# Kernel optimization log

Hardware: AMD Instinct MI355X
Metric: run time of the kernel (lower is better)

## Reference

```python
import jax, jax.numpy as jnp
import numpy as np

N_NODES = 100000
N_EDGES = 600000
DIM = 128
N_BEHAVIORS = 4


def setup_inputs() -> dict:
    key = jax.random.key(0)
    ks = jax.random.split(key, 10)
    user = jax.random.randint(ks[0], (N_NODES,), 0, N_NODES, dtype=jnp.int32)
    item = jax.random.randint(ks[1], (N_NODES,), 0, N_NODES, dtype=jnp.int32)
    behavior = jax.random.randint(ks[2], (N_NODES,), 0, N_BEHAVIORS, dtype=jnp.int32)
    adj_rows = jax.random.randint(ks[3], (N_EDGES,), 0, N_NODES, dtype=jnp.int32)
    adj_cols = jax.random.randint(ks[4], (N_EDGES,), 0, N_NODES, dtype=jnp.int32)
    adj_vals = jax.random.uniform(ks[5], (N_EDGES,), dtype=jnp.float32)
    user_table = jax.random.normal(ks[6], (N_NODES, DIM), dtype=jnp.float32)
    item_table = jax.random.normal(ks[7], (N_NODES, DIM), dtype=jnp.float32)
    behavior_table = jax.random.normal(ks[8], (N_BEHAVIORS, DIM), dtype=jnp.float32)
    kw, kb = jax.random.split(ks[9])
    bound = 1.0 / np.sqrt(DIM)
    W = jax.random.uniform(kw, (DIM, DIM), minval=-bound, maxval=bound, dtype=jnp.float32)
    b = jax.random.uniform(kb, (DIM,), minval=-bound, maxval=bound, dtype=jnp.float32)
    return {"user": user, "item": item, "behavior": behavior,
            "adj_rows": adj_rows, "adj_cols": adj_cols, "adj_vals": adj_vals,
            "user_table": user_table, "item_table": item_table,
            "behavior_table": behavior_table, "W": W, "b": b}


def reference(user, item, behavior, adj_rows, adj_cols, adj_vals,
              user_table, item_table, behavior_table, W, b):
    # embedding sum: [N, D]
    x = user_table[user] + item_table[item] + behavior_table[behavior]
    # sparse adjacency matmul: out[r] = sum_e adj_vals[e] * x[cols[e]] for rows[e]==r
    msg = adj_vals[:, None] * x[adj_cols]                       # [E, D]
    agg = jax.ops.segment_sum(msg, adj_rows, num_segments=N_NODES)  # [N, D]
    # dense linear
    return agg @ W.T + b
```

## Files before the change

### kernel.cpp

```cpp
#include <hip/hip_runtime.h>

#define N_NODES 100000
#define N_EDGES 600000
#define DIM 128

#define N4 (N_NODES / 4)
#define SCAN_BLOCKS ((N_NODES + 1023) / 1024)

typedef __attribute__((ext_vector_type(8))) short bf16x8;
typedef __attribute__((ext_vector_type(4))) float f32x4;

__device__ __forceinline__ void fma4(float4& acc, float s, const float4 w) {
    acc.x = fmaf(s, w.x, acc.x);
    acc.y = fmaf(s, w.y, acc.y);
    acc.z = fmaf(s, w.z, acc.z);
    acc.w = fmaf(s, w.w, acc.w);
}

__device__ __forceinline__ unsigned short f2bf(float f) {
    union { float f; unsigned int u; } v; v.f = f;
    unsigned int r = v.u + 0x7fffu + ((v.u >> 16) & 1u);
    return (unsigned short)(r >> 16);
}

__device__ __forceinline__ float bf2f(unsigned short u) {
    union { unsigned int i; float f; } v;
    v.i = ((unsigned int)u) << 16;
    return v.f;
}

__global__ __launch_bounds__(256) void hist_kernel(
    const int* __restrict__ rows, int* __restrict__ cnt)
{
    int e = blockIdx.x * 256 + threadIdx.x;
    if (e >= N_EDGES) return;
    atomicAdd(&cnt[rows[e]], 1);
}

__global__ __launch_bounds__(256) void scan1_kernel(
    const int* __restrict__ cnt, int* __restrict__ off, int* __restrict__ bsum)
{
    __shared__ int s[256];
    int t = threadIdx.x;
    int b = blockIdx.x;
    int i4 = b * 256 + t;
    int4 c = {0, 0, 0, 0};
    if (i4 < N4) c = ((const int4*)cnt)[i4];
    int tsum = c.x + c.y + c.z + c.w;
    s[t] = tsum;
    __syncthreads();
    for (int d = 1; d < 256; d <<= 1) {
        int v = (t >= d) ? s[t - d] : 0;
        __syncthreads();
        s[t] += v;
        __syncthreads();
    }
    int texcl = s[t] - tsum;
    if (t == 255) bsum[b] = s[255];
    if (i4 < N4) {
        int4 o;
        o.x = texcl;
        o.y = o.x + c.x;
        o.z = o.y + c.y;
        o.w = o.z + c.z;
        ((int4*)off)[i4] = o;
    }
}

__global__ __launch_bounds__(256) void scan3_kernel(
    const int* __restrict__ bsum, int* __restrict__ off, int* __restrict__ cur)
{
    __shared__ int s[256];
    int t = threadIdx.x;
    int b = blockIdx.x;
    s[t] = (t < b && t < SCAN_BLOCKS) ? bsum[t] : 0;
    __syncthreads();
    for (int d = 1; d < 256; d <<= 1) {
        int v = (t >= d) ? s[t - d] : 0;
        __syncthreads();
        s[t] += v;
        __syncthreads();
    }
    int base = s[255];
    int i4 = b * 256 + t;
    if (i4 < N4) {
        int4 o = ((const int4*)off)[i4];
        o.x += base; o.y += base; o.z += base; o.w += base;
        ((int4*)off)[i4] = o;
        ((int4*)cur)[i4] = o;
    }
    if (b == 0 && t == 0) off[N_NODES] = N_EDGES;
}

__global__ __launch_bounds__(256) void bucket_kernel(
    const int* __restrict__ rows, const int* __restrict__ cols, const float* __restrict__ vals,
    int* __restrict__ cur, int2* __restrict__ epack)
{
    int e = blockIdx.x * 256 + threadIdx.x;
    if (e >= N_EDGES) return;
    int r = rows[e];
    int slot = atomicAdd(&cur[r], 1);
    int2 p;
    p.x = cols[e];
    p.y = __float_as_int(vals[e]);
    epack[slot] = p;
}

__global__ __launch_bounds__(256) void wconv_kernel(
    const float* __restrict__ W, unsigned short* __restrict__ wfrag)
{
    int c4 = blockIdx.x * 256 + threadIdx.x;
    if (c4 >= 128 * 128 / 4) return;
    float4 wv = ((const float4*)W)[c4];
    int i  = c4 >> 5;
    int k0 = (c4 & 31) * 4;
    int slot = (i >> 4) * 4 + (k0 >> 5);
    int lane = ((k0 & 31) >> 3) * 16 + (i & 15);
    ushort4 o;
    o.x = f2bf(wv.x); o.y = f2bf(wv.y); o.z = f2bf(wv.z); o.w = f2bf(wv.w);
    *(ushort4*)&wfrag[slot * 512 + lane * 8 + (k0 & 7)] = o;
}

__global__ __launch_bounds__(256, 6) void fused_embed_gemm_kernel(
    const int* __restrict__ user, const int* __restrict__ item, const int* __restrict__ behavior,
    const float* __restrict__ ut, const float* __restrict__ itb, const float* __restrict__ bt,
    const bf16x8* __restrict__ wf, unsigned short* __restrict__ y)
{
    int tid = threadIdx.x;
    int l = tid & 63;
    int w = tid >> 6;
    int c = l & 15;
    int g = l >> 4;
    int row = blockIdx.x * 64 + w * 16 + c;
    int rowc = row < N_NODES ? row : N_NODES - 1;

    int u  = user[rowc];
    int iv = item[rowc];
    int bh = behavior[rowc];
    const float4* ut4 = (const float4*)ut;
    const float4* it4 = (const float4*)itb;
    const float4* bt4 = (const float4*)bt;

    bf16x8 bfrag[4];
    #pragma unroll
    for (int s = 0; s < 4; ++s) {
        int base = 8 * s + 2 * g;
        float4 a0 = ut4[(size_t)u  * 32 + base];
        float4 a1 = ut4[(size_t)u  * 32 + base + 1];
        float4 c0 = it4[(size_t)iv * 32 + base];
        float4 c1 = it4[(size_t)iv * 32 + base + 1];
        float4 d0 = bt4[(size_t)bh * 32 + base];
        float4 d1 = bt4[(size_t)bh * 32 + base + 1];
        bf16x8 t;
        t[0] = (short)f2bf(a0.x + c0.x + d0.x);
        t[1] = (short)f2bf(a0.y + c0.y + d0.y);
        t[2] = (short)f2bf(a0.z + c0.z + d0.z);
        t[3] = (short)f2bf(a0.w + c0.w + d0.w);
        t[4] = (short)f2bf(a1.x + c1.x + d1.x);
        t[5] = (short)f2bf(a1.y + c1.y + d1.y);
        t[6] = (short)f2bf(a1.z + c1.z + d1.z);
        t[7] = (short)f2bf(a1.w + c1.w + d1.w);
        bfrag[s] = t;
    }

    f32x4 acc[8];
    #pragma unroll
    for (int ti = 0; ti < 8; ++ti) acc[ti] = (f32x4){0.f, 0.f, 0.f, 0.f};

    #pragma unroll
    for (int ti = 0; ti < 8; ++ti) {
        #pragma unroll
        for (int s = 0; s < 4; ++s) {
            bf16x8 af = wf[(ti * 4 + s) * 64 + l];
            acc[ti] = __builtin_amdgcn_mfma_f32_16x16x32_bf16(af, bfrag[s], acc[ti], 0, 0, 0);
        }
    }

    if (row < N_NODES) {
        unsigned short* yr = y + (size_t)row * DIM;
        #pragma unroll
        for (int ti = 0; ti < 8; ++ti) {
            ushort4 o;
            o.x = f2bf(acc[ti][0]);
            o.y = f2bf(acc[ti][1]);
            o.z = f2bf(acc[ti][2]);
            o.w = f2bf(acc[ti][3]);
            *(ushort4*)(yr + 16 * ti + 4 * g) = o;
        }
    }
}

__global__ __launch_bounds__(256) void agg_bias_kernel(
    const int* __restrict__ off, const int2* __restrict__ epack,
    const unsigned short* __restrict__ y, const float* __restrict__ bias,
    float* __restrict__ out)
{
    int gid = blockIdx.x * 256 + threadIdx.x;
    int r = gid >> 4;
    int m = gid & 15;
    if (r >= N_NODES) return;
    int s = off[r], e = off[r + 1];
    const bf16x8* y8 = (const bf16x8*)y;

    float a0[8], a1[8];
    #pragma unroll
    for (int j = 0; j < 8; ++j) { a0[j] = 0.f; a1[j] = 0.f; }

    int i = s;
    for (; i + 1 < e; i += 2) {
        int2 p0 = epack[i];
        int2 p1 = epack[i + 1];
        float v0 = __int_as_float(p0.y);
        float v1 = __int_as_float(p1.y);
        bf16x8 ya = y8[(size_t)p0.x * 16 + m];
        bf16x8 yb = y8[(size_t)p1.x * 16 + m];
        #pragma unroll
        for (int j = 0; j < 8; ++j) {
            a0[j] = fmaf(v0, bf2f((unsigned short)ya[j]), a0[j]);
            a1[j] = fmaf(v1, bf2f((unsigned short)yb[j]), a1[j]);
        }
    }
    if (i < e) {
        int2 p0 = epack[i];
        float v0 = __int_as_float(p0.y);
        bf16x8 ya = y8[(size_t)p0.x * 16 + m];
        #pragma unroll
        for (int j = 0; j < 8; ++j)
            a0[j] = fmaf(v0, bf2f((unsigned short)ya[j]), a0[j]);
    }

    const float4* b4 = (const float4*)bias;
    float4 bb0 = b4[2 * m], bb1 = b4[2 * m + 1];
    float4 o0, o1;
    o0.x = a0[0] + a1[0] + bb0.x;
    o0.y = a0[1] + a1[1] + bb0.y;
    o0.z = a0[2] + a1[2] + bb0.z;
    o0.w = a0[3] + a1[3] + bb0.w;
    o1.x = a0[4] + a1[4] + bb1.x;
    o1.y = a0[5] + a1[5] + bb1.y;
    o1.z = a0[6] + a1[6] + bb1.z;
    o1.w = a0[7] + a1[7] + bb1.w;
    float4* orow = (float4*)(out + (size_t)r * DIM);
    orow[2 * m]     = o0;
    orow[2 * m + 1] = o1;
}


__global__ __launch_bounds__(256) void agg_fused_kernel(
    const int* __restrict__ off, const int2* __restrict__ epack,
    const int* __restrict__ user, const int* __restrict__ item, const int* __restrict__ behavior,
    const float* __restrict__ ut, const float* __restrict__ itb, const float* __restrict__ bt,
    float* __restrict__ out)
{
    int gid = blockIdx.x * 256 + threadIdx.x;
    int r = gid >> 5;
    int m = gid & 31;
    if (r >= N_NODES) return;
    int s = off[r], e = off[r + 1];
    const float4* ut4 = (const float4*)ut;
    const float4* it4 = (const float4*)itb;
    const float4* bt4 = (const float4*)bt;
    float4 acc = {0.f, 0.f, 0.f, 0.f};
    for (int i = s; i < e; ++i) {
        int2 p = epack[i];
        int c = p.x;
        float v = __int_as_float(p.y);
        float4 a = ut4[(size_t)user[c] * 32 + m];
        float4 cc = it4[(size_t)item[c] * 32 + m];
        float4 d = bt4[(size_t)behavior[c] * 32 + m];
        a.x += cc.x + d.x; a.y += cc.y + d.y; a.z += cc.z + d.z; a.w += cc.w + d.w;
        fma4(acc, v, a);
    }
    ((float4*)out)[(size_t)r * 32 + m] = acc;
}

__global__ __launch_bounds__(256) void scatter_fused_kernel(
    const int* __restrict__ rows, const int* __restrict__ cols, const float* __restrict__ vals,
    const int* __restrict__ user, const int* __restrict__ item, const int* __restrict__ behavior,
    const float* __restrict__ ut, const float* __restrict__ itb, const float* __restrict__ bt,
    float* __restrict__ agg)
{
    int wave = (blockIdx.x * 256 + threadIdx.x) >> 6;
    int lane = threadIdx.x & 63;
    int e = wave * 2 + (lane >> 5);
    if (e >= N_EDGES) return;
    int r = rows[e];
    int c = cols[e];
    float v = vals[e];
    int m = lane & 31;
    const float4* ut4 = (const float4*)ut;
    const float4* it4 = (const float4*)itb;
    const float4* bt4 = (const float4*)bt;
    float4 a = ut4[(size_t)user[c] * 32 + m];
    float4 cc = it4[(size_t)item[c] * 32 + m];
    float4 d = bt4[(size_t)behavior[c] * 32 + m];
    a.x += cc.x + d.x; a.y += cc.y + d.y; a.z += cc.z + d.z; a.w += cc.w + d.w;
    float* o = agg + (size_t)r * DIM + m * 4;
    atomicAdd(o + 0, v * a.x);
    atomicAdd(o + 1, v * a.y);
    atomicAdd(o + 2, v * a.z);
    atomicAdd(o + 3, v * a.w);
}

__global__ __launch_bounds__(256) void gemm_mfma_kernel(
    const float* __restrict__ W, const float* __restrict__ bias, float* io)
{
    __shared__ unsigned short wlds[128 * 128];

    int tid = threadIdx.x;
    for (int c4 = tid; c4 < 128 * 128 / 4; c4 += 256) {
        float4 wv = ((const float4*)W)[c4];
        int i  = c4 >> 5;
        int k0 = (c4 & 31) * 4;
        int slot = (i >> 4) * 4 + (k0 >> 5);
        int lane = ((k0 & 31) >> 3) * 16 + (i & 15);
        ushort4 o;
        o.x = f2bf(wv.x); o.y = f2bf(wv.y); o.z = f2bf(wv.z); o.w = f2bf(wv.w);
        *(ushort4*)&wlds[slot * 512 + lane * 8 + (k0 & 7)] = o;
    }
    __syncthreads();

    int l = tid & 63;
    int w = tid >> 6;
    int c = l & 15;
    int g = l >> 4;
    int r0 = blockIdx.x * 64 + w * 16;
    int row = r0 + c;
    int rowc = row < N_NODES ? row : N_NODES - 1;

    const float4* a4 = (const float4*)io;
    bf16x8 bfrag[4];
    #pragma unroll
    for (int s = 0; s < 4; ++s) {
        float4 p0 = a4[(size_t)rowc * 32 + 8 * s + 2 * g];
        float4 p1 = a4[(size_t)rowc * 32 + 8 * s + 2 * g + 1];
        bf16x8 t;
        t[0] = (short)f2bf(p0.x); t[1] = (short)f2bf(p0.y);
        t[2] = (short)f2bf(p0.z); t[3] = (short)f2bf(p0.w);
        t[4] = (short)f2bf(p1.x); t[5] = (short)f2bf(p1.y);
        t[6] = (short)f2bf(p1.z); t[7] = (short)f2bf(p1.w);
        bfrag[s] = t;
    }

    f32x4 acc[8];
    #pragma unroll
    for (int ti = 0; ti < 8; ++ti) acc[ti] = (f32x4){0.f, 0.f, 0.f, 0.f};

    const bf16x8* wf = (const bf16x8*)wlds;
    #pragma unroll
    for (int ti = 0; ti < 8; ++ti) {
        #pragma unroll
        for (int s = 0; s < 4; ++s) {
            bf16x8 af = wf[(ti * 4 + s) * 64 + l];
            acc[ti] = __builtin_amdgcn_mfma_f32_16x16x32_bf16(af, bfrag[s], acc[ti], 0, 0, 0);
        }
    }

    if (row < N_NODES) {
        float4* orow = (float4*)(io + (size_t)row * DIM);
        const float4* b4 = (const float4*)bias;
        #pragma unroll
        for (int ti = 0; ti < 8; ++ti) {
            float4 bb = b4[ti * 4 + g];
            float4 o;
            o.x = acc[ti][0] + bb.x;
            o.y = acc[ti][1] + bb.y;
            o.z = acc[ti][2] + bb.z;
            o.w = acc[ti][3] + bb.w;
            orow[ti * 4 + g] = o;
        }
    }
}

extern "C" void kernel_launch(void* const* d_in, const int* in_sizes, int n_in,
                              void* d_out, int out_size, void* d_ws, size_t ws_size,
                              hipStream_t stream) {
    const int*   user           = (const int*)d_in[0];
    const int*   item           = (const int*)d_in[1];
    const int*   behavior       = (const int*)d_in[2];
    const int*   adj_rows       = (const int*)d_in[3];
    const int*   adj_cols       = (const int*)d_in[4];
    const float* adj_vals       = (const float*)d_in[5];
    const float* user_table     = (const float*)d_in[6];
    const float* item_table     = (const float*)d_in[7];
    const float* behavior_table = (const float*)d_in[8];
    const float* W              = (const float*)d_in[9];
    const float* b              = (const float*)d_in[10];
    float* out = (float*)d_out;

    const size_t Y_BYTES     = (size_t)N_NODES * DIM * sizeof(unsigned short);
    const size_t CNT_BYTES   = (size_t)N_NODES * sizeof(int);
    const size_t OFF_BYTES   = ((size_t)(N_NODES + 1) * sizeof(int) + 15) & ~(size_t)15;
    const size_t EPACK_BYTES = (size_t)N_EDGES * sizeof(int2);
    const size_t WFRAG_BYTES = 128 * 128 * sizeof(unsigned short);

    const int edge_blocks = (N_EDGES + 255) / 256;
    const int fused_blocks = (N_NODES + 63) / 64;
    const int gemm_blocks = (N_NODES + 63) / 64;
    const int agg_blocks  = (N_NODES * 16 + 255) / 256;

    char* ws = (char*)d_ws;
    const size_t need_full = Y_BYTES + CNT_BYTES + OFF_BYTES + EPACK_BYTES + WFRAG_BYTES;
    const size_t need_csr  = CNT_BYTES + OFF_BYTES + EPACK_BYTES;

    if (ws_size >= need_full) {
        unsigned short* y = (unsigned short*)ws;
        int*  cnt   = (int*)(ws + Y_BYTES);
        int*  off   = (int*)(ws + Y_BYTES + CNT_BYTES);
        int2* epack = (int2*)(ws + Y_BYTES + CNT_BYTES + OFF_BYTES);
        unsigned short* wfrag = (unsigned short*)(ws + Y_BYTES + CNT_BYTES + OFF_BYTES + EPACK_BYTES);
        int*  bsum  = (int*)epack;

        hipMemsetAsync(cnt, 0, CNT_BYTES, stream);
        wconv_kernel<<<16, 256, 0, stream>>>(W, wfrag);
        hist_kernel<<<edge_blocks, 256, 0, stream>>>(adj_rows, cnt);
        scan1_kernel<<<SCAN_BLOCKS, 256, 0, stream>>>(cnt, off, bsum);
        scan3_kernel<<<SCAN_BLOCKS, 256, 0, stream>>>(bsum, off, cnt);
        bucket_kernel<<<edge_blocks, 256, 0, stream>>>(
            adj_rows, adj_cols, adj_vals, cnt, epack);
        fused_embed_gemm_kernel<<<fused_blocks, 256, 0, stream>>>(
            user, item, behavior, user_table, item_table, behavior_table,
            (const bf16x8*)wfrag, y);
        agg_bias_kernel<<<agg_blocks, 256, 0, stream>>>(off, epack, y, b, out);
    } else if (ws_size >= need_csr) {
        int*  cnt   = (int*)ws;
        int*  off   = (int*)(ws + CNT_BYTES);
        int2* epack = (int2*)(ws + CNT_BYTES + OFF_BYTES);
        int*  bsum  = (int*)epack;

        hipMemsetAsync(cnt, 0, CNT_BYTES, stream);
        hist_kernel<<<edge_blocks, 256, 0, stream>>>(adj_rows, cnt);
        scan1_kernel<<<SCAN_BLOCKS, 256, 0, stream>>>(cnt, off, bsum);
        scan3_kernel<<<SCAN_BLOCKS, 256, 0, stream>>>(bsum, off, cnt);
        bucket_kernel<<<edge_blocks, 256, 0, stream>>>(
            adj_rows, adj_cols, adj_vals, cnt, epack);
        agg_fused_kernel<<<(N_NODES * 32 + 255) / 256, 256, 0, stream>>>(
            off, epack, user, item, behavior,
            user_table, item_table, behavior_table, out);
        gemm_mfma_kernel<<<gemm_blocks, 256, 0, stream>>>(W, b, out);
    } else {
        hipMemsetAsync(d_out, 0, (size_t)N_NODES * DIM * sizeof(float), stream);
        const int scatter_blocks = (N_EDGES / 2 * 64 + 255) / 256;
        scatter_fused_kernel<<<scatter_blocks, 256, 0, stream>>>(
            adj_rows, adj_cols, adj_vals, user, item, behavior,
            user_table, item_table, behavior_table, out);
        gemm_mfma_kernel<<<gemm_blocks, 256, 0, stream>>>(W, b, out);
    }
}
```

Baseline: 146.7 us.

## Merge independent stages into multi-role kernels and unroll aggregation by four

The old fused embed+GEMM kernel is split into two parts. The embedding sum now runs in one combined kernel alongside the edge histogram and the weight conversion. The GEMM runs in place on the bf16 embedding buffer in a persistent kernel that also does the CSR bucketing, with W staged in shared memory. Fewer launches let independent work overlap, and the aggregation loop now keeps four edges in flight instead of two. The cost is an extra bf16 round trip of X through memory, plus 32KB of LDS per GEMM block, which may limit occupancy.

```diff
diff --git a/kernel.cpp b/kernel.cpp
--- a/kernel.cpp
+++ b/kernel.cpp
@@ -6,6 +6,13 @@
 
 #define N4 (N_NODES / 4)
 #define SCAN_BLOCKS ((N_NODES + 1023) / 1024)
+
+#define EMBED_B 6250
+#define HIST_B  2344
+#define WCONV_B 16
+#define GEMM_B   782
+#define BUCKET_B 2344
+#define NTILES   1563
 
 typedef __attribute__((ext_vector_type(8))) short bf16x8;
 typedef __attribute__((ext_vector_type(4))) float f32x4;
@@ -29,12 +36,58 @@
     return v.f;
 }
 
-__global__ __launch_bounds__(256) void hist_kernel(
-    const int* __restrict__ rows, int* __restrict__ cnt)
-{
-    int e = blockIdx.x * 256 + threadIdx.x;
-    if (e >= N_EDGES) return;
-    atomicAdd(&cnt[rows[e]], 1);
+__global__ __launch_bounds__(256) void k1_kernel(
+    const int* __restrict__ user, const int* __restrict__ item, const int* __restrict__ behavior,
+    const float* __restrict__ ut, const float* __restrict__ itb, const float* __restrict__ bt,
+    const int* __restrict__ rows, const float* __restrict__ W,
+    unsigned short* __restrict__ x16, int* __restrict__ cnt, unsigned short* __restrict__ wfrag)
+{
+    int b = blockIdx.x;
+    int t = threadIdx.x;
+    if (b < EMBED_B) {
+        int gid = b * 256 + t;
+        int r = gid >> 4;
+        int m = gid & 15;
+        int u  = user[r];
+        int iv = item[r];
+        int bh = behavior[r];
+        const float4* ut4 = (const float4*)ut;
+        const float4* it4 = (const float4*)itb;
+        const float4* bt4 = (const float4*)bt;
+        float4 a0 = ut4[(size_t)u  * 32 + 2 * m];
+        float4 a1 = ut4[(size_t)u  * 32 + 2 * m + 1];
+        float4 c0 = it4[(size_t)iv * 32 + 2 * m];
+        float4 c1 = it4[(size_t)iv * 32 + 2 * m + 1];
+        float4 d0 = bt4[(size_t)bh * 32 + 2 * m];
+        float4 d1 = bt4[(size_t)bh * 32 + 2 * m + 1];
+        ushort4 o0, o1;
+        o0.x = f2bf(a0.x + c0.x + d0.x);
+        o0.y = f2bf(a0.y + c0.y + d0.y);
+        o0.z = f2bf(a0.z + c0.z + d0.z);
+        o0.w = f2bf(a0.w + c0.w + d0.w);
+        o1.x = f2bf(a1.x + c1.x + d1.x);
+        o1.y = f2bf(a1.y + c1.y + d1.y);
+        o1.z = f2bf(a1.z + c1.z + d1.z);
+        o1.w = f2bf(a1.w + c1.w + d1.w);
+        unsigned short* xr = x16 + (size_t)r * DIM + 8 * m;
+        *(ushort4*)xr       = o0;
+        *(ushort4*)(xr + 4) = o1;
+    } else if (b < EMBED_B + HIST_B) {
+        int e = (b - EMBED_B) * 256 + t;
+        if (e < N_EDGES) atomicAdd(&cnt[rows[e]], 1);
+    } else {
+        int c4 = (b - EMBED_B - HIST_B) * 256 + t;
+        if (c4 < 128 * 128 / 4) {
+            float4 wv = ((const float4*)W)[c4];
+            int i  = c4 >> 5;
+            int k0 = (c4 & 31) * 4;
+            int slot = (i >> 4) * 4 + (k0 >> 5);
+            int lane = ((k0 & 31) >> 3) * 16 + (i & 15);
+            ushort4 o;
+            o.x = f2bf(wv.x); o.y = f2bf(wv.y); o.z = f2bf(wv.z); o.w = f2bf(wv.w);
+            *(ushort4*)&wfrag[slot * 512 + lane * 8 + (k0 & 7)] = o;
+        }
+    }
 }
 
 __global__ __launch_bounds__(256) void scan1_kernel(
@@ -92,6 +145,144 @@
     if (b == 0 && t == 0) off[N_NODES] = N_EDGES;
 }
 
+__global__ __launch_bounds__(256) void k4_kernel(
+    const unsigned short* __restrict__ wfrag, unsigned short* xy,
+    const int* __restrict__ rows, const int* __restrict__ cols, const float* __restrict__ vals,
+    int* __restrict__ cur, int2* __restrict__ epack)
+{
+    __shared__ unsigned short wl[128 * 128];
+    int b = blockIdx.x;
+    int t = threadIdx.x;
+    if (b < GEMM_B) {
+        for (int i = t; i < 2048; i += 256)
+            ((float4*)wl)[i] = ((const float4*)wfrag)[i];
+        __syncthreads();
+
+        int l = t & 63;
+        int w = t >> 6;
+        int c = l & 15;
+        int g = l >> 4;
+        const bf16x8* wf = (const bf16x8*)wl;
+
+        for (int bt = b; bt < NTILES; bt += GEMM_B) {
+            int row = bt * 64 + w * 16 + c;
+            int rowc = row < N_NODES ? row : N_NODES - 1;
+            const bf16x8* xr = (const bf16x8*)(xy + (size_t)rowc * DIM);
+            bf16x8 bfrag[4];
+            #pragma unroll
+            for (int s = 0; s < 4; ++s) bfrag[s] = xr[g + 4 * s];
+
+            f32x4 acc[8];
+            #pragma unroll
+            for (int ti = 0; ti < 8; ++ti) acc[ti] = (f32x4){0.f, 0.f, 0.f, 0.f};
+
+            #pragma unroll
+            for (int ti = 0; ti < 8; ++ti) {
+                #pragma unroll
+                for (int s = 0; s < 4; ++s) {
+                    bf16x8 af = wf[(ti * 4 + s) * 64 + l];
+                    acc[ti] = __builtin_amdgcn_mfma_f32_16x16x32_bf16(af, bfrag[s], acc[ti], 0, 0, 0);
+                }
+            }
+
+            if (row < N_NODES) {
+                unsigned short* yr = xy + (size_t)row * DIM;
+                #pragma unroll
+                for (int ti = 0; ti < 8; ++ti) {
+                    ushort4 o;
+                    o.x = f2bf(acc[ti][0]);
+                    o.y = f2bf(acc[ti][1]);
+                    o.z = f2bf(acc[ti][2]);
+                    o.w = f2bf(acc[ti][3]);
+                    *(ushort4*)(yr + 16 * ti + 4 * g) = o;
+                }
+            }
+        }
+    } else {
+        int e = (b - GEMM_B) * 256 + t;
+        if (e < N_EDGES) {
+            int r = rows[e];
+            int slot = atomicAdd(&cur[r], 1);
+            int2 p;
+            p.x = cols[e];
+            p.y = __float_as_int(vals[e]);
+            epack[slot] = p;
+        }
+    }
+}
+
+__global__ __launch_bounds__(256) void agg_bias_kernel(
+    const int* __restrict__ off, const int2* __restrict__ epack,
+    const unsigned short* __restrict__ y, const float* __restrict__ bias,
+    float* __restrict__ out)
+{
+    int gid = blockIdx.x * 256 + threadIdx.x;
+    int r = gid >> 4;
+    int m = gid & 15;
+    if (r >= N_NODES) return;
+    int s = off[r], e = off[r + 1];
+    const bf16x8* y8 = (const bf16x8*)y;
+
+    float a0[8], a1[8], a2[8], a3[8];
+    #pragma unroll
+    for (int j = 0; j < 8; ++j) { a0[j] = 0.f; a1[j] = 0.f; a2[j] = 0.f; a3[j] = 0.f; }
+
+    int i = s;
+    for (; i + 3 < e; i += 4) {
+        int2 p0 = epack[i];
+        int2 p1 = epack[i + 1];
+        int2 p2 = epack[i + 2];
+        int2 p3 = epack[i + 3];
+        bf16x8 y0 = y8[(size_t)p0.x * 16 + m];
+        bf16x8 y1 = y8[(size_t)p1.x * 16 + m];
+        bf16x8 y2 = y8[(size_t)p2.x * 16 + m];
+        bf16x8 y3 = y8[(size_t)p3.x * 16 + m];
+        float v0 = __int_as_float(p0.y);
+        float v1 = __int_as_float(p1.y);
+        float v2 = __int_as_float(p2.y);
+        float v3 = __int_as_float(p3.y);
+        #pragma unroll
+        for (int j = 0; j < 8; ++j) {
+            a0[j] = fmaf(v0, bf2f((unsigned short)y0[j]), a0[j]);
+            a1[j] = fmaf(v1, bf2f((unsigned short)y1[j]), a1[j]);
+            a2[j] = fmaf(v2, bf2f((unsigned short)y2[j]), a2[j]);
+            a3[j] = fmaf(v3, bf2f((unsigned short)y3[j]), a3[j]);
+        }
+    }
+    for (; i < e; ++i) {
+        int2 p0 = epack[i];
+        float v0 = __int_as_float(p0.y);
+        bf16x8 y0 = y8[(size_t)p0.x * 16 + m];
+        #pragma unroll
+        for (int j = 0; j < 8; ++j)
+            a0[j] = fmaf(v0, bf2f((unsigned short)y0[j]), a0[j]);
+    }
+
+    const float4* b4 = (const float4*)bias;
+    float4 bb0 = b4[2 * m], bb1 = b4[2 * m + 1];
+    float4 o0, o1;
+    o0.x = a0[0] + a1[0] + a2[0] + a3[0] + bb0.x;
+    o0.y = a0[1] + a1[1] + a2[1] + a3[1] + bb0.y;
+    o0.z = a0[2] + a1[2] + a2[2] + a3[2] + bb0.z;
+    o0.w = a0[3] + a1[3] + a2[3] + a3[3] + bb0.w;
+    o1.x = a0[4] + a1[4] + a2[4] + a3[4] + bb1.x;
+    o1.y = a0[5] + a1[5] + a2[5] + a3[5] + bb1.y;
+    o1.z = a0[6] + a1[6] + a2[6] + a3[6] + bb1.z;
+    o1.w = a0[7] + a1[7] + a2[7] + a3[7] + bb1.w;
+    float4* orow = (float4*)(out + (size_t)r * DIM);
+    orow[2 * m]     = o0;
+    orow[2 * m + 1] = o1;
+}
+
+
+__global__ __launch_bounds__(256) void hist_kernel(
+    const int* __restrict__ rows, int* __restrict__ cnt)
+{
+    int e = blockIdx.x * 256 + threadIdx.x;
+    if (e >= N_EDGES) return;
+    atomicAdd(&cnt[rows[e]], 1);
+}
+
 __global__ __launch_bounds__(256) void bucket_kernel(
     const int* __restrict__ rows, const int* __restrict__ cols, const float* __restrict__ vals,
     int* __restrict__ cur, int2* __restrict__ epack)
@@ -105,146 +296,6 @@
     p.y = __float_as_int(vals[e]);
     epack[slot] = p;
 }
-
-__global__ __launch_bounds__(256) void wconv_kernel(
-    const float* __restrict__ W, unsigned short* __restrict__ wfrag)
-{
-    int c4 = blockIdx.x * 256 + threadIdx.x;
-    if (c4 >= 128 * 128 / 4) return;
-    float4 wv = ((const float4*)W)[c4];
-    int i  = c4 >> 5;
-    int k0 = (c4 & 31) * 4;
-    int slot = (i >> 4) * 4 + (k0 >> 5);
-    int lane = ((k0 & 31) >> 3) * 16 + (i & 15);
-    ushort4 o;
-    o.x = f2bf(wv.x); o.y = f2bf(wv.y); o.z = f2bf(wv.z); o.w = f2bf(wv.w);
-    *(ushort4*)&wfrag[slot * 512 + lane * 8 + (k0 & 7)] = o;
-}
-
-__global__ __launch_bounds__(256, 6) void fused_embed_gemm_kernel(
-    const int* __restrict__ user, const int* __restrict__ item, const int* __restrict__ behavior,
-    const float* __restrict__ ut, const float* __restrict__ itb, const float* __restrict__ bt,
-    const bf16x8* __restrict__ wf, unsigned short* __restrict__ y)
-{
-    int tid = threadIdx.x;
-    int l = tid & 63;
-    int w = tid >> 6;
-    int c = l & 15;
-    int g = l >> 4;
-    int row = blockIdx.x * 64 + w * 16 + c;
-    int rowc = row < N_NODES ? row : N_NODES - 1;
-
-    int u  = user[rowc];
-    int iv = item[rowc];
-    int bh = behavior[rowc];
-    const float4* ut4 = (const float4*)ut;
-    const float4* it4 = (const float4*)itb;
-    const float4* bt4 = (const float4*)bt;
-
-    bf16x8 bfrag[4];
-    #pragma unroll
-    for (int s = 0; s < 4; ++s) {
-        int base = 8 * s + 2 * g;
-        float4 a0 = ut4[(size_t)u  * 32 + base];
-        float4 a1 = ut4[(size_t)u  * 32 + base + 1];
-        float4 c0 = it4[(size_t)iv * 32 + base];
-        float4 c1 = it4[(size_t)iv * 32 + base + 1];
-        float4 d0 = bt4[(size_t)bh * 32 + base];
-        float4 d1 = bt4[(size_t)bh * 32 + base + 1];
-        bf16x8 t;
-        t[0] = (short)f2bf(a0.x + c0.x + d0.x);
-        t[1] = (short)f2bf(a0.y + c0.y + d0.y);
-        t[2] = (short)f2bf(a0.z + c0.z + d0.z);
-        t[3] = (short)f2bf(a0.w + c0.w + d0.w);
-        t[4] = (short)f2bf(a1.x + c1.x + d1.x);
-        t[5] = (short)f2bf(a1.y + c1.y + d1.y);
-        t[6] = (short)f2bf(a1.z + c1.z + d1.z);
-        t[7] = (short)f2bf(a1.w + c1.w + d1.w);
-        bfrag[s] = t;
-    }
-
-    f32x4 acc[8];
-    #pragma unroll
-    for (int ti = 0; ti < 8; ++ti) acc[ti] = (f32x4){0.f, 0.f, 0.f, 0.f};
-
-    #pragma unroll
-    for (int ti = 0; ti < 8; ++ti) {
-        #pragma unroll
-        for (int s = 0; s < 4; ++s) {
-            bf16x8 af = wf[(ti * 4 + s) * 64 + l];
-            acc[ti] = __builtin_amdgcn_mfma_f32_16x16x32_bf16(af, bfrag[s], acc[ti], 0, 0, 0);
-        }
-    }
-
-    if (row < N_NODES) {
-        unsigned short* yr = y + (size_t)row * DIM;
-        #pragma unroll
-        for (int ti = 0; ti < 8; ++ti) {
-            ushort4 o;
-            o.x = f2bf(acc[ti][0]);
-            o.y = f2bf(acc[ti][1]);
-            o.z = f2bf(acc[ti][2]);
-            o.w = f2bf(acc[ti][3]);
-            *(ushort4*)(yr + 16 * ti + 4 * g) = o;
-        }
-    }
-}
-
-__global__ __launch_bounds__(256) void agg_bias_kernel(
-    const int* __restrict__ off, const int2* __restrict__ epack,
-    const unsigned short* __restrict__ y, const float* __restrict__ bias,
-    float* __restrict__ out)
-{
-    int gid = blockIdx.x * 256 + threadIdx.x;
-    int r = gid >> 4;
-    int m = gid & 15;
-    if (r >= N_NODES) return;
-    int s = off[r], e = off[r + 1];
-    const bf16x8* y8 = (const bf16x8*)y;
-
-    float a0[8], a1[8];
-    #pragma unroll
-    for (int j = 0; j < 8; ++j) { a0[j] = 0.f; a1[j] = 0.f; }
-
-    int i = s;
-    for (; i + 1 < e; i += 2) {
-        int2 p0 = epack[i];
-        int2 p1 = epack[i + 1];
-        float v0 = __int_as_float(p0.y);
-        float v1 = __int_as_float(p1.y);
-        bf16x8 ya = y8[(size_t)p0.x * 16 + m];
-        bf16x8 yb = y8[(size_t)p1.x * 16 + m];
-        #pragma unroll
-        for (int j = 0; j < 8; ++j) {
-            a0[j] = fmaf(v0, bf2f((unsigned short)ya[j]), a0[j]);
-            a1[j] = fmaf(v1, bf2f((unsigned short)yb[j]), a1[j]);
-        }
-    }
-    if (i < e) {
-        int2 p0 = epack[i];
-        float v0 = __int_as_float(p0.y);
-        bf16x8 ya = y8[(size_t)p0.x * 16 + m];
-        #pragma unroll
-        for (int j = 0; j < 8; ++j)
-            a0[j] = fmaf(v0, bf2f((unsigned short)ya[j]), a0[j]);
-    }
-
-    const float4* b4 = (const float4*)bias;
-    float4 bb0 = b4[2 * m], bb1 = b4[2 * m + 1];
-    float4 o0, o1;
-    o0.x = a0[0] + a1[0] + bb0.x;
-    o0.y = a0[1] + a1[1] + bb0.y;
-    o0.z = a0[2] + a1[2] + bb0.z;
-    o0.w = a0[3] + a1[3] + bb0.w;
-    o1.x = a0[4] + a1[4] + bb1.x;
-    o1.y = a0[5] + a1[5] + bb1.y;
-    o1.z = a0[6] + a1[6] + bb1.z;
-    o1.w = a0[7] + a1[7] + bb1.w;
-    float4* orow = (float4*)(out + (size_t)r * DIM);
-    orow[2 * m]     = o0;
-    orow[2 * m + 1] = o1;
-}
-
 
 __global__ __launch_bounds__(256) void agg_fused_kernel(
     const int* __restrict__ off, const int2* __restrict__ epack,
@@ -324,8 +375,7 @@
     int w = tid >> 6;
     int c = l & 15;
     int g = l >> 4;
-    int r0 = blockIdx.x * 64 + w * 16;
-    int row = r0 + c;
+    int row = blockIdx.x * 64 + w * 16 + c;
     int rowc = row < N_NODES ? row : N_NODES - 1;
 
     const float4* a4 = (const float4*)io;
@@ -388,40 +438,37 @@
     const float* b              = (const float*)d_in[10];
     float* out = (float*)d_out;
 
-    const size_t Y_BYTES     = (size_t)N_NODES * DIM * sizeof(unsigned short);
+    const size_t X16_BYTES   = (size_t)N_NODES * DIM * sizeof(unsigned short);
     const size_t CNT_BYTES   = (size_t)N_NODES * sizeof(int);
     const size_t OFF_BYTES   = ((size_t)(N_NODES + 1) * sizeof(int) + 15) & ~(size_t)15;
     const size_t EPACK_BYTES = (size_t)N_EDGES * sizeof(int2);
     const size_t WFRAG_BYTES = 128 * 128 * sizeof(unsigned short);
 
     const int edge_blocks = (N_EDGES + 255) / 256;
-    const int fused_blocks = (N_NODES + 63) / 64;
+    const int agg_blocks  = (N_NODES * 16 + 255) / 256;
     const int gemm_blocks = (N_NODES + 63) / 64;
-    const int agg_blocks  = (N_NODES * 16 + 255) / 256;
 
     char* ws = (char*)d_ws;
-    const size_t need_full = Y_BYTES + CNT_BYTES + OFF_BYTES + EPACK_BYTES + WFRAG_BYTES;
+    const size_t need_full = X16_BYTES + CNT_BYTES + OFF_BYTES + EPACK_BYTES + WFRAG_BYTES;
     const size_t need_csr  = CNT_BYTES + OFF_BYTES + EPACK_BYTES;
 
     if (ws_size >= need_full) {
-        unsigned short* y = (unsigned short*)ws;
-        int*  cnt   = (int*)(ws + Y_BYTES);
-        int*  off   = (int*)(ws + Y_BYTES + CNT_BYTES);
-        int2* epack = (int2*)(ws + Y_BYTES + CNT_BYTES + OFF_BYTES);
-        unsigned short* wfrag = (unsigned short*)(ws + Y_BYTES + CNT_BYTES + OFF_BYTES + EPACK_BYTES);
+        unsigned short* x16 = (unsigned short*)ws;
+        int*  cnt   = (int*)(ws + X16_BYTES);
+        int*  off   = (int*)(ws + X16_BYTES + CNT_BYTES);
+        int2* epack = (int2*)(ws + X16_BYTES + CNT_BYTES + OFF_BYTES);
+        unsigned short* wfrag = (unsigned short*)(ws + X16_BYTES + CNT_BYTES + OFF_BYTES + EPACK_BYTES);
         int*  bsum  = (int*)epack;
 
         hipMemsetAsync(cnt, 0, CNT_BYTES, stream);
-        wconv_kernel<<<16, 256, 0, stream>>>(W, wfrag);
-        hist_kernel<<<edge_blocks, 256, 0, stream>>>(adj_rows, cnt);
+        k1_kernel<<<EMBED_B + HIST_B + WCONV_B, 256, 0, stream>>>(
+            user, item, behavior, user_table, item_table, behavior_table,
+            adj_rows, W, x16, cnt, wfrag);
         scan1_kernel<<<SCAN_BLOCKS, 256, 0, stream>>>(cnt, off, bsum);
         scan3_kernel<<<SCAN_BLOCKS, 256, 0, stream>>>(bsum, off, cnt);
-        bucket_kernel<<<edge_blocks, 256, 0, stream>>>(
-            adj_rows, adj_cols, adj_vals, cnt, epack);
-        fused_embed_gemm_kernel<<<fused_blocks, 256, 0, stream>>>(
-            user, item, behavior, user_table, item_table, behavior_table,
-            (const bf16x8*)wfrag, y);
-        agg_bias_kernel<<<agg_blocks, 256, 0, stream>>>(off, epack, y, b, out);
+        k4_kernel<<<GEMM_B + BUCKET_B, 256, 0, stream>>>(
+            wfrag, x16, adj_rows, adj_cols, adj_vals, cnt, epack);
+        agg_bias_kernel<<<agg_blocks, 256, 0, stream>>>(off, epack, x16, b, out);
     } else if (ws_size >= need_csr) {
         int*  cnt   = (int*)ws;
         int*  off   = (int*)(ws + CNT_BYTES);
```

Result: faster. 137.2 us (-6.5%).
